# Performance work log

Measured on AMD Instinct MI355X. Metric: run time of the kernel, lower is better.

The kernel has to match this reference:

```python
import jax, jax.numpy as jnp
import numpy as np

NEG_SLOPE = 0.2  # PyG GATConv default LeakyReLU slope
EPS = 1e-16      # PyG softmax denominator epsilon


def _gat_layer(x, src, dst, W, a_src, a_dst, b, H, C):
    """One PyG-style GATConv layer (eval mode, add_self_loops already applied).
    x: [N, F_in], W: [F_in, H*C], a_src/a_dst: [H, C], b: [H*C]."""
    N = x.shape[0]
    h = (x @ W).reshape(N, H, C)                       # [N,H,C]
    alpha_src = jnp.sum(h * a_src, axis=-1)            # [N,H]
    alpha_dst = jnp.sum(h * a_dst, axis=-1)            # [N,H]
    e = jax.nn.leaky_relu(alpha_src[src] + alpha_dst[dst], NEG_SLOPE)  # [E,H]
    m = jax.ops.segment_max(e, dst, num_segments=N)    # [N,H] segment-softmax max
    p = jnp.exp(e - m[dst])                            # [E,H]
    s = jax.ops.segment_sum(p, dst, num_segments=N)    # [N,H]
    attn = p / (s[dst] + EPS)                          # [E,H]
    out = jax.ops.segment_sum(attn[:, :, None] * h[src], dst, num_segments=N)  # [N,H,C]
    return out.reshape(N, H * C) + b


def _add_self_loops(edge_index, N):
    loop = jnp.arange(N, dtype=edge_index.dtype)
    src = jnp.concatenate([edge_index[0], loop])
    dst = jnp.concatenate([edge_index[1], loop])
    return src, dst


def setup_inputs() -> dict:
    key = jax.random.key(0)
    N, E = 50000, 500000
    F_in, H, C = 336, 4, 128
    HC = H * C  # 512
    n_cls = 10
    ks = jax.random.split(key, 16)

    def glorot(k, shape):
        fan = shape[0] + shape[-1]
        return jax.random.normal(k, shape, jnp.float32) * jnp.sqrt(2.0 / fan)

    x = jax.random.normal(ks[0], (N, F_in), jnp.float32)
    edge_index = jax.random.randint(ks[1], (2, E), 0, N, dtype=jnp.int64)
    return {
        "x": x,
        "edge_index": edge_index,
        "W1": glorot(ks[2], (F_in, HC)),
        "a_src1": glorot(ks[3], (H, C)),
        "a_dst1": glorot(ks[4], (H, C)),
        "b1": jnp.zeros((HC,), jnp.float32),
        "W2": glorot(ks[5], (HC, HC)),
        "a_src2": glorot(ks[6], (H, C)),
        "a_dst2": glorot(ks[7], (H, C)),
        "b2": jnp.zeros((HC,), jnp.float32),
        "Wc1": glorot(ks[8], (HC, C)),
        "bc1": jnp.zeros((C,), jnp.float32),
        "Wc2": glorot(ks[9], (C, n_cls)),
        "bc2": jnp.zeros((n_cls,), jnp.float32),
    }


def reference(x, edge_index, W1, a_src1, a_dst1, b1, W2, a_src2, a_dst2, b2, Wc1, bc1, Wc2, bc2):
    H, C = 4, 128
    N = x.shape[0]
    src, dst = _add_self_loops(edge_index, N)
    h = _gat_layer(x, src, dst, W1, a_src1, a_dst1, b1, H, C)
    h = jax.nn.elu(h)  # ELU between layers only
    h = _gat_layer(h, src, dst, W2, a_src2, a_dst2, b2, H, C)
    # classifier (dropout is identity in eval)
    z = jax.nn.relu(h @ Wc1 + bc1)
    logits = z @ Wc2 + bc2
    return logits
```

## Files before the change

kernel.cpp:

```cpp
#include <hip/hip_runtime.h>
#include <math.h>

typedef unsigned short u16;
typedef unsigned int u32;
typedef short short8 __attribute__((ext_vector_type(8)));
typedef __bf16 bf16x8 __attribute__((ext_vector_type(8)));
typedef float f32x4 __attribute__((ext_vector_type(4)));
typedef u32 u32x4 __attribute__((ext_vector_type(4)));

typedef const __attribute__((address_space(1))) void* as1cv;
typedef __attribute__((address_space(3))) void* as3v;

__device__ __forceinline__ void gload16(const void* g, void* l) {
    __builtin_amdgcn_global_load_lds((as1cv)g, (as3v)l, 16, 0, 0);
}

__device__ __forceinline__ float b2f(u16 u) {
    union { u32 i; float f; } v; v.i = ((u32)u) << 16; return v.f;
}
__device__ __forceinline__ float b2f_lo(u32 q) {
    union { u32 i; float f; } v; v.i = q << 16; return v.f;
}
__device__ __forceinline__ float b2f_hi(u32 q) {
    union { u32 i; float f; } v; v.i = q & 0xffff0000u; return v.f;
}
__device__ __forceinline__ u16 f2b(float f) {
    union { float f; u32 i; } v; v.f = f;
    u32 i = v.i;
    u32 r = (i + 0x7fffu + ((i >> 16) & 1u)) >> 16;
    return (u16)r;
}
__device__ __forceinline__ u32 pack2(u16 a, u16 b) { return (u32)a | ((u32)b << 16); }


__device__ void agg_dev(const int* __restrict__ rowptr, const int* __restrict__ col,
                        const float* __restrict__ asrc, const float* __restrict__ adst,
                        const u16* __restrict__ hb, const float* __restrict__ bias,
                        u16* __restrict__ outb, int elu, int NODES) {
    const int wid = __builtin_amdgcn_readfirstlane((blockIdx.x * 256 + threadIdx.x) >> 6);
    const int nwaves = gridDim.x << 2;
    const int l = threadIdx.x & 63;
    const int hd = l >> 4;
    const int cbase = 8 * l;
    float bv[8];
#pragma unroll
    for (int c = 0; c < 8; c++) bv[c] = bias[cbase + c];

    for (int n = wid; n < NODES; n += nwaves) {
        const int beg = __builtin_amdgcn_readfirstlane(rowptr[n]);
        const int end = __builtin_amdgcn_readfirstlane(rowptr[n + 1]);
        const float ad = adst[n * 4 + hd];
        float acc0[8], acc1[8];
#pragma unroll
        for (int c = 0; c < 8; c++) { acc0[c] = 0.f; acc1[c] = 0.f; }
        float ss0 = 0.f, ss1 = 0.f;
        for (int j = beg; j < end; j += 8) {
            int s[8];
#pragma unroll
            for (int q = 0; q < 8; q++) {
                int jq = j + q;
                jq = jq < end ? jq : end - 1;
                s[q] = __builtin_amdgcn_readfirstlane(col[jq]);
            }
            u32x4 g[8];
#pragma unroll
            for (int q = 0; q < 8; q++)
                g[q] = *(const u32x4*)(hb + (size_t)s[q] * 512 + cbase);
            float p[8];
#pragma unroll
            for (int q = 0; q < 8; q++) {
                float e = asrc[(size_t)s[q] * 4 + hd] + ad;
                e = e > 0.f ? e : 0.2f * e;
                float pe = __expf(e);
                p[q] = (j + q < end) ? pe : 0.f;
            }
#pragma unroll
            for (int q = 0; q < 8; q += 2) {
                ss0 += p[q]; ss1 += p[q + 1];
#pragma unroll
                for (int u = 0; u < 4; u++) {
                    acc0[2 * u]     += p[q]     * b2f_lo(g[q][u]);
                    acc0[2 * u + 1] += p[q]     * b2f_hi(g[q][u]);
                    acc1[2 * u]     += p[q + 1] * b2f_lo(g[q + 1][u]);
                    acc1[2 * u + 1] += p[q + 1] * b2f_hi(g[q + 1][u]);
                }
            }
        }
        float inv = 1.f / (ss0 + ss1 + 1e-16f);
        float v[8];
#pragma unroll
        for (int c = 0; c < 8; c++) {
            float tv = (acc0[c] + acc1[c]) * inv + bv[c];
            if (elu) tv = tv > 0.f ? tv : expm1f(tv);
            v[c] = tv;
        }
        u32x4 ov;
        ov[0] = pack2(f2b(v[0]), f2b(v[1]));
        ov[1] = pack2(f2b(v[2]), f2b(v[3]));
        ov[2] = pack2(f2b(v[4]), f2b(v[5]));
        ov[3] = pack2(f2b(v[6]), f2b(v[7]));
        *(u32x4*)(outb + (size_t)n * 512 + cbase) = ov;
    }
}

__device__ void gemm_dev(const u16* __restrict__ A, const u16* __restrict__ Bt,
                         u16* __restrict__ C, const float* __restrict__ bias,
                         const float* __restrict__ aS, const float* __restrict__ aD,
                         float* __restrict__ asr, float* __restrict__ ads,
                         const float* __restrict__ Wc2, const float* __restrict__ bc2,
                         float* __restrict__ outp,
                         int M, int N, int K, int act, char* shm,
                         u16* As0, u16* As1, u16* Bs0, u16* Bs1,
                         float (*red)[128][2]) {
    const int t = threadIdx.x;
    const int l = t & 63, w = t >> 6;

    const int nwg = gridDim.x * gridDim.y;
    const int fid = blockIdx.x + gridDim.x * blockIdx.y;
    int logical;
    {
        const int q = nwg >> 3, r = nwg & 7;
        const int xcd = fid & 7, ix = fid >> 3;
        logical = (xcd < r ? xcd * (q + 1) : r * (q + 1) + (xcd - r) * q) + ix;
    }
    const int gy = gridDim.y;
    const int mtile = logical / gy;
    const int hd_ = logical - mtile * gy;
    const int m0 = mtile * 128, n0 = hd_ * 128;

    const int wm = (w >> 1) * 64, wn = (w & 1) * 64;

    const int rl0 = w * 32 + (l >> 2);
    const int rl1 = rl0 + 16;
    const int gso = 8 * ((l & 3) ^ ((l >> 3) & 3));
    const u16* pA0 = A + (size_t)min(m0 + rl0, M - 1) * K + gso;
    const u16* pA1 = A + (size_t)min(m0 + rl1, M - 1) * K + gso;
    const u16* pB0 = Bt + (size_t)min(n0 + rl0, N - 1) * K + gso;
    const u16* pB1 = Bt + (size_t)min(n0 + rl1, N - 1) * K + gso;
    const int wbase = (w * 32) * 32;

    const int rs = ((l & 15) >> 1) & 3;
    const int roff = 8 * ((l >> 4) ^ rs);

    f32x4 acc[4][4];
    f32x4 z4 = {0.f, 0.f, 0.f, 0.f};
#pragma unroll
    for (int i = 0; i < 4; i++)
#pragma unroll
        for (int j = 0; j < 4; j++) acc[i][j] = z4;

    auto STAGE = [&](u16* As_, u16* Bs_, int k0) {
        gload16(pA0 + k0, As_ + wbase);
        gload16(pA1 + k0, As_ + wbase + 16 * 32);
        gload16(pB0 + k0, Bs_ + wbase);
        gload16(pB1 + k0, Bs_ + wbase + 16 * 32);
    };
    auto COMP = [&](const u16* As_, const u16* Bs_) {
        bf16x8 af[4], bfr[4];
#pragma unroll
        for (int i = 0; i < 4; i++) {
            af[i]  = *(const bf16x8*)(As_ + (wm + i * 16 + (l & 15)) * 32 + roff);
            bfr[i] = *(const bf16x8*)(Bs_ + (wn + i * 16 + (l & 15)) * 32 + roff);
        }
        __builtin_amdgcn_s_setprio(1);
#pragma unroll
        for (int i = 0; i < 4; i++)
#pragma unroll
            for (int j = 0; j < 4; j++)
                acc[i][j] = __builtin_amdgcn_mfma_f32_16x16x32_bf16(af[i], bfr[j], acc[i][j], 0, 0, 0);
        __builtin_amdgcn_s_setprio(0);
    };

    const int ns = K >> 5;
    STAGE(As0, Bs0, 0);
    __syncthreads();
    int s = 0;
    while (true) {
        if (s + 1 < ns) STAGE(As1, Bs1, (s + 1) << 5);
        COMP(As0, Bs0);
        __syncthreads();
        if (++s >= ns) break;
        if (s + 1 < ns) STAGE(As0, Bs0, (s + 1) << 5);
        COMP(As1, Bs1);
        __syncthreads();
        if (++s >= ns) break;
    }

    if (act == 2) {
        float* wl = (float*)shm;
        float (*logbuf)[128][10] = (float (*)[128][10])(shm + 8192);
        for (int i = t; i < 1280; i += 256) wl[i] = Wc2[i];
        if (t < 10) wl[1280 + t] = bc2[t];
        __syncthreads();
        int cj[4];
#pragma unroll
        for (int j = 0; j < 4; j++) cj[j] = wn + j * 16 + (l & 15);
#pragma unroll
        for (int i = 0; i < 4; i++) {
#pragma unroll
            for (int r = 0; r < 4; r++) {
                float zv[4];
#pragma unroll
                for (int j = 0; j < 4; j++) {
                    float v = acc[i][j][r] + (bias ? bias[cj[j]] : 0.f);
                    zv[j] = v > 0.f ? v : 0.f;
                }
                float part[10];
#pragma unroll
                for (int k = 0; k < 10; k++) {
                    float s2 = 0.f;
#pragma unroll
                    for (int j = 0; j < 4; j++) s2 += zv[j] * wl[cj[j] * 10 + k];
#pragma unroll
                    for (int o = 1; o < 16; o <<= 1) s2 += __shfl_xor(s2, o);
                    part[k] = s2;
                }
                if ((l & 15) == 0) {
                    int rl = wm + i * 16 + (l >> 4) * 4 + r;
#pragma unroll
                    for (int k = 0; k < 10; k++) logbuf[w & 1][rl][k] = part[k];
                }
            }
        }
        __syncthreads();
        if (t < 128) {
            int row = m0 + t;
            if (row < M) {
#pragma unroll
                for (int k = 0; k < 10; k++)
                    outp[(size_t)row * 10 + k] =
                        logbuf[0][t][k] + logbuf[1][t][k] + wl[1280 + k];
            }
        }
        return;
    }

#pragma unroll
    for (int i = 0; i < 4; i++) {
        int rbase = m0 + wm + i * 16 + (l >> 4) * 4;
#pragma unroll
        for (int j = 0; j < 4; j++) {
            int c = n0 + wn + j * 16 + (l & 15);
            float bv = bias ? bias[c] : 0.f;
#pragma unroll
            for (int r = 0; r < 4; r++) {
                int row = rbase + r;
                if (row < M) {
                    float v = acc[i][j][r] + bv;
                    if (act == 1) v = v > 0.f ? v : 0.f;
                    C[(size_t)row * N + c] = f2b(v);
                }
            }
        }
    }

    if (aS) {
        const int hd = n0 >> 7;
        float aSv[4], aDv[4];
#pragma unroll
        for (int j = 0; j < 4; j++) {
            int c = n0 + wn + j * 16 + (l & 15);
            aSv[j] = aS[c];
            aDv[j] = aD[c];
        }
#pragma unroll
        for (int i = 0; i < 4; i++) {
#pragma unroll
            for (int r = 0; r < 4; r++) {
                float vs = 0.f, vd = 0.f;
#pragma unroll
                for (int j = 0; j < 4; j++) {
                    float hv = acc[i][j][r];
                    vs += hv * aSv[j];
                    vd += hv * aDv[j];
                }
#pragma unroll
                for (int o = 1; o < 16; o <<= 1) {
                    vs += __shfl_xor(vs, o);
                    vd += __shfl_xor(vd, o);
                }
                if ((l & 15) == 0) {
                    int rl = wm + i * 16 + (l >> 4) * 4 + r;
                    red[w & 1][rl][0] = vs;
                    red[w & 1][rl][1] = vd;
                }
            }
        }
        __syncthreads();
        if (t < 128) {
            int row = m0 + t;
            if (row < M) {
                asr[row * 4 + hd] = red[0][t][0] + red[1][t][0];
                ads[row * 4 + hd] = red[0][t][1] + red[1][t][1];
            }
        }
    }
}

__global__ __launch_bounds__(256) void BaselineGAT_41764261987077_kernel(
    int phase, int aux,
    const float* x, const int* ei,
    const float* W1, const float* as1, const float* ad1, const float* b1,
    const float* W2, const float* as2, const float* ad2, const float* b2,
    const float* Wc1, const float* bc1, const float* Wc2, const float* bc2,
    float* out,
    u16* hAb, u16* hbB, float* asr, float* ads,
    u16* xb, u16* w1t, u16* w2t, u16* wc1t,
    int* flag, int* cnt, int* tmp, int* bsum, int* boff,
    int* rowptr, int* cursor, int* col,
    const u16* gA, const u16* gB, u16* gC, const float* gBias,
    const float* gAs, const float* gAd,
    int gM, int gN, int gK, int gAct,
    int NODES, int E, int nblk)
{
    __shared__ f32x4 shm4[2176];
    char* shm = (char*)shm4;
    u16* As0 = (u16*)shm;
    u16* As1 = (u16*)(shm + 8192);
    u16* Bs0 = (u16*)(shm + 16384);
    u16* Bs1 = (u16*)(shm + 24576);
    float (*red)[128][2] = (float (*)[128][2])(shm + 32768);
    int* smi = (int*)shm;
    int* smb = (int*)(shm + 2048);

    const int t = threadIdx.x;
    const int gid = blockIdx.x * 256 + t;
    const int EN = E + NODES;

    switch (phase) {
    case 100: {
        if (gid < NODES * 10) out[gid] = 1000.0f;
    } break;
    case 0: {
        if (blockIdx.x == 0) {
            if (t == 0) smi[256] = 0;
            __syncthreads();
            for (int j = t; j < 1024; j += 256)
                if (ei[2 * j + 1] != 0) atomicAdd(&smi[256], 1);
            __syncthreads();
            if (t == 0) flag[0] = (smi[256] < 16) ? 2 : 1;
        } else {
            int i = (blockIdx.x - 1) * 256 + t;
            if (i < NODES) cnt[i] = 0;
        }
    } break;
    case 2: {
        if (gid >= EN) return;
        int step = flag[0];
        int d;
        if (gid < E) {
            d = ei[(size_t)(E + gid) * step];
            if ((unsigned)d >= (unsigned)NODES) d = 0;
        } else d = gid - E;
        atomicAdd(&cnt[d], 1);
    } break;
    case 3: {
        smi[t] = (gid < NODES) ? cnt[gid] : 0;
        __syncthreads();
        for (int o = 1; o < 256; o <<= 1) {
            int add = (t >= o) ? smi[t - o] : 0;
            __syncthreads();
            smi[t] += add;
            __syncthreads();
        }
        if (gid < NODES) tmp[gid] = smi[t];
        if (t == 255) bsum[blockIdx.x] = smi[255];
    } break;
    case 5: {
        smb[t] = (t < nblk) ? bsum[t] : 0;
        __syncthreads();
        for (int o = 1; o < 256; o <<= 1) {
            int add = (t >= o) ? smb[t - o] : 0;
            __syncthreads();
            smb[t] += add;
            __syncthreads();
        }
        int base = (blockIdx.x == 0) ? 0 : smb[blockIdx.x - 1];
        if (gid >= NODES) return;
        int incl = tmp[gid] + base;
        rowptr[gid + 1] = incl;
        cursor[gid] = incl - cnt[gid];
        if (gid == 0) rowptr[0] = 0;
    } break;
    case 6: {
        if (gid >= EN) return;
        int step = flag[0];
        int d, s;
        if (gid < E) {
            s = ei[(size_t)gid * step];
            d = ei[(size_t)(E + gid) * step];
            if ((unsigned)s >= (unsigned)NODES) s = 0;
            if ((unsigned)d >= (unsigned)NODES) d = 0;
        } else { d = gid - E; s = d; }
        int pos = atomicAdd(&cursor[d], 1);
        col[pos] = s;
    } break;
    case 20: {
        int i = gid;
        const int XC = NODES * 44;
        if (i < XC) {
            int n = i / 44, kk = (i - n * 44) * 8;
            short8 o;
            if (kk < 336) {
                const f32x4* xp = (const f32x4*)(x + (size_t)n * 336 + kk);
                f32x4 f0 = xp[0], f1 = xp[1];
                o[0] = (short)f2b(f0[0]); o[1] = (short)f2b(f0[1]);
                o[2] = (short)f2b(f0[2]); o[3] = (short)f2b(f0[3]);
                o[4] = (short)f2b(f1[0]); o[5] = (short)f2b(f1[1]);
                o[6] = (short)f2b(f1[2]); o[7] = (short)f2b(f1[3]);
            } else {
#pragma unroll
                for (int e = 0; e < 8; e++) o[e] = 0;
            }
            *(short8*)(xb + (size_t)n * 352 + kk) = o;
            return;
        }
        i -= XC;
        if (i < 512 * 352) {
            int n = i / 352, k = i - n * 352;
            w1t[i] = (k < 336) ? f2b(W1[(size_t)k * 512 + n]) : (u16)0;
            return;
        }
        i -= 512 * 352;
        if (i < 512 * 512) {
            int n = i >> 9, k = i & 511;
            w2t[i] = f2b(W2[(size_t)k * 512 + n]);
            return;
        }
        i -= 512 * 512;
        if (i < 128 * 512) {
            int n = i >> 9, k = i & 511;
            wc1t[i] = f2b(Wc1[(size_t)k * 128 + n]);
        }
    } break;
    case 30: gemm_dev(gA, gB, gC, gBias, gAs, gAd, asr, ads,
                      Wc2, bc2, out, gM, gN, gK, gAct, shm,
                      As0, As1, Bs0, Bs1, red); break;
    case 31: agg_dev(rowptr, col, asr, ads, hAb, gBias, hbB, aux, NODES); break;
    }
}

extern "C" void kernel_launch(void* const* d_in, const int* in_sizes, int n_in,
                              void* d_out, int out_size, void* d_ws, size_t ws_size,
                              hipStream_t stream) {
    const float* x   = (const float*)d_in[0];
    const int*   ei  = (const int*)d_in[1];
    const float* W1  = (const float*)d_in[2];
    const float* as1 = (const float*)d_in[3];
    const float* ad1 = (const float*)d_in[4];
    const float* b1  = (const float*)d_in[5];
    const float* W2  = (const float*)d_in[6];
    const float* as2 = (const float*)d_in[7];
    const float* ad2 = (const float*)d_in[8];
    const float* b2  = (const float*)d_in[9];
    const float* Wc1 = (const float*)d_in[10];
    const float* bc1 = (const float*)d_in[11];
    const float* Wc2 = (const float*)d_in[12];
    const float* bc2 = (const float*)d_in[13];

    const int NODES = in_sizes[0] / 336;
    const int E     = in_sizes[1] / 2;

    char* ws = (char*)d_ws;
    size_t off = 0;
    auto alloc = [&](size_t b) -> char* {
        char* p = ws + off; off = (off + b + 255) & ~(size_t)255; return p;
    };
    u16*   xb   = (u16*)alloc((size_t)NODES * 352 * 2);
    u16*   hAb  = (u16*)alloc((size_t)NODES * 512 * 2);
    u16*   hbB  = (u16*)alloc((size_t)NODES * 512 * 2);
    float* asr  = (float*)alloc((size_t)NODES * 4 * 4);
    float* ads  = (float*)alloc((size_t)NODES * 4 * 4);
    u16*   w1t  = (u16*)alloc((size_t)512 * 352 * 2);
    u16*   w2t  = (u16*)alloc((size_t)512 * 512 * 2);
    u16*   wc1t = (u16*)alloc((size_t)128 * 512 * 2);
    int* flag   = (int*)alloc(256);
    int* cnt    = (int*)alloc((size_t)NODES * 4);
    int* tmp    = (int*)alloc((size_t)NODES * 4);
    int* bsum   = (int*)alloc(4096);
    int* boff   = (int*)alloc(4096);
    int* rowptr = (int*)alloc((size_t)(NODES + 1) * 4);
    int* cursor = (int*)alloc((size_t)NODES * 4);
    int* col    = (int*)alloc((size_t)(E + NODES) * 4);

    const int nblk = (NODES + 255) / 256;
    const int eblk = (E + NODES + 255) / 256;
    const int oblk = (out_size + 255) / 256;
    const int mt   = (NODES + 127) / 128;
    const int cvt_total = NODES * 44 + 512 * 352 + 512 * 512 + 128 * 512;

    auto L = [&](int phase, int aux, dim3 grid,
                 const u16* gA = nullptr, const u16* gB = nullptr,
                 u16* gC = nullptr, const float* gBias = nullptr,
                 const float* gAs = nullptr, const float* gAd = nullptr,
                 int gM = 0, int gN = 0, int gK = 0, int gAct = 0) {
        BaselineGAT_41764261987077_kernel<<<grid, 256, 0, stream>>>(
            phase, aux, x, ei, W1, as1, ad1, b1, W2, as2, ad2, b2,
            Wc1, bc1, Wc2, bc2, (float*)d_out,
            hAb, hbB, asr, ads, xb, w1t, w2t, wc1t,
            flag, cnt, tmp, bsum, boff, rowptr, cursor, col,
            gA, gB, gC, gBias, gAs, gAd, gM, gN, gK, gAct,
            NODES, E, nblk);
    };

    if (n_in < 14 || off > ws_size) { L(100, 1, oblk); return; }

    L(0, 0, nblk + 1);
    L(2, 0, eblk);
    L(3, 0, nblk);
    L(5, 0, nblk);
    L(6, 0, eblk);

    L(20, 0, (cvt_total + 255) / 256);

    L(30, 0, dim3(mt, 4), xb, w1t, hAb, nullptr, as1, ad1, NODES, 512, 352, 0);
    L(31, 1, 4096, nullptr, nullptr, nullptr, b1);

    L(30, 0, dim3(mt, 4), hbB, w2t, hAb, nullptr, as2, ad2, NODES, 512, 512, 0);
    L(31, 0, 4096, nullptr, nullptr, nullptr, b2);

    L(30, 0, dim3(mt, 1), hbB, wc1t, nullptr, bc1, nullptr, nullptr, NODES, 128, 512, 2);
}
```

Before: 576.5 us.

## Triple-buffer GEMM K-loop with vmcnt-based waits and dynamic shared memory

```diff
diff --git a/kernel.cpp b/kernel.cpp
--- a/kernel.cpp
+++ b/kernel.cpp
@@ -109,11 +109,16 @@
                          float* __restrict__ asr, float* __restrict__ ads,
                          const float* __restrict__ Wc2, const float* __restrict__ bc2,
                          float* __restrict__ outp,
-                         int M, int N, int K, int act, char* shm,
-                         u16* As0, u16* As1, u16* Bs0, u16* Bs1,
-                         float (*red)[128][2]) {
+                         int M, int N, int K, int act, char* shm) {
     const int t = threadIdx.x;
     const int l = t & 63, w = t >> 6;
+
+    u16* As0 = (u16*)shm;
+    u16* As1 = (u16*)(shm + 8192);
+    u16* As2 = (u16*)(shm + 16384);
+    u16* Bs0 = (u16*)(shm + 24576);
+    u16* Bs1 = (u16*)(shm + 32768);
+    u16* Bs2 = (u16*)(shm + 40960);
 
     const int nwg = gridDim.x * gridDim.y;
     const int fid = blockIdx.x + gridDim.x * blockIdx.y;
@@ -170,19 +175,30 @@
                 acc[i][j] = __builtin_amdgcn_mfma_f32_16x16x32_bf16(af[i], bfr[j], acc[i][j], 0, 0, 0);
         __builtin_amdgcn_s_setprio(0);
     };
+    auto WSEL = [&](int s_, int ns_) {
+        int ahead = ns_ - 1 - s_;
+        if (ahead >= 2)      asm volatile("s_waitcnt vmcnt(8)" ::: "memory");
+        else if (ahead == 1) asm volatile("s_waitcnt vmcnt(4)" ::: "memory");
+        else                 asm volatile("s_waitcnt vmcnt(0)" ::: "memory");
+    };
 
     const int ns = K >> 5;
     STAGE(As0, Bs0, 0);
-    __syncthreads();
+    STAGE(As1, Bs1, 32);
+    STAGE(As2, Bs2, 64);
     int s = 0;
     while (true) {
-        if (s + 1 < ns) STAGE(As1, Bs1, (s + 1) << 5);
-        COMP(As0, Bs0);
-        __syncthreads();
+        WSEL(s, ns); __builtin_amdgcn_s_barrier();
+        COMP(As0, Bs0); __builtin_amdgcn_s_barrier();
+        if (s + 3 < ns) STAGE(As0, Bs0, (s + 3) << 5);
         if (++s >= ns) break;
-        if (s + 1 < ns) STAGE(As0, Bs0, (s + 1) << 5);
-        COMP(As1, Bs1);
-        __syncthreads();
+        WSEL(s, ns); __builtin_amdgcn_s_barrier();
+        COMP(As1, Bs1); __builtin_amdgcn_s_barrier();
+        if (s + 3 < ns) STAGE(As1, Bs1, (s + 3) << 5);
+        if (++s >= ns) break;
+        WSEL(s, ns); __builtin_amdgcn_s_barrier();
+        COMP(As2, Bs2); __builtin_amdgcn_s_barrier();
+        if (s + 3 < ns) STAGE(As2, Bs2, (s + 3) << 5);
         if (++s >= ns) break;
     }
 
@@ -255,6 +271,7 @@
     }
 
     if (aS) {
+        float (*red)[128][2] = (float (*)[128][2])shm;
         const int hd = n0 >> 7;
         float aSv[4], aDv[4];
 #pragma unroll
@@ -313,15 +330,10 @@
     int gM, int gN, int gK, int gAct,
     int NODES, int E, int nblk)
 {
-    __shared__ f32x4 shm4[2176];
-    char* shm = (char*)shm4;
-    u16* As0 = (u16*)shm;
-    u16* As1 = (u16*)(shm + 8192);
-    u16* Bs0 = (u16*)(shm + 16384);
-    u16* Bs1 = (u16*)(shm + 24576);
-    float (*red)[128][2] = (float (*)[128][2])(shm + 32768);
-    int* smi = (int*)shm;
-    int* smb = (int*)(shm + 2048);
+    __shared__ int sstat[1024];
+    extern __shared__ char dynshm[];
+    int* smi = sstat;
+    int* smb = sstat + 512;
 
     const int t = threadIdx.x;
     const int gid = blockIdx.x * 256 + t;
@@ -434,8 +446,7 @@
         }
     } break;
     case 30: gemm_dev(gA, gB, gC, gBias, gAs, gAd, asr, ads,
-                      Wc2, bc2, out, gM, gN, gK, gAct, shm,
-                      As0, As1, Bs0, Bs1, red); break;
+                      Wc2, bc2, out, gM, gN, gK, gAct, dynshm); break;
     case 31: agg_dev(rowptr, col, asr, ads, hAb, gBias, hbB, aux, NODES); break;
     }
 }
@@ -489,12 +500,12 @@
     const int mt   = (NODES + 127) / 128;
     const int cvt_total = NODES * 44 + 512 * 352 + 512 * 512 + 128 * 512;
 
-    auto L = [&](int phase, int aux, dim3 grid,
+    auto L = [&](int phase, int aux, dim3 grid, size_t shmem,
                  const u16* gA = nullptr, const u16* gB = nullptr,
                  u16* gC = nullptr, const float* gBias = nullptr,
                  const float* gAs = nullptr, const float* gAd = nullptr,
                  int gM = 0, int gN = 0, int gK = 0, int gAct = 0) {
-        BaselineGAT_41764261987077_kernel<<<grid, 256, 0, stream>>>(
+        BaselineGAT_41764261987077_kernel<<<grid, 256, shmem, stream>>>(
             phase, aux, x, ei, W1, as1, ad1, b1, W2, as2, ad2, b2,
             Wc1, bc1, Wc2, bc2, (float*)d_out,
             hAb, hbB, asr, ads, xb, w1t, w2t, wc1t,
@@ -502,22 +513,23 @@
             gA, gB, gC, gBias, gAs, gAd, gM, gN, gK, gAct,
             NODES, E, nblk);
     };
-
-    if (n_in < 14 || off > ws_size) { L(100, 1, oblk); return; }
-
-    L(0, 0, nblk + 1);
-    L(2, 0, eblk);
-    L(3, 0, nblk);
-    L(5, 0, nblk);
-    L(6, 0, eblk);
-
-    L(20, 0, (cvt_total + 255) / 256);
-
-    L(30, 0, dim3(mt, 4), xb, w1t, hAb, nullptr, as1, ad1, NODES, 512, 352, 0);
-    L(31, 1, 4096, nullptr, nullptr, nullptr, b1);
-
-    L(30, 0, dim3(mt, 4), hbB, w2t, hAb, nullptr, as2, ad2, NODES, 512, 512, 0);
-    L(31, 0, 4096, nullptr, nullptr, nullptr, b2);
-
-    L(30, 0, dim3(mt, 1), hbB, wc1t, nullptr, bc1, nullptr, nullptr, NODES, 128, 512, 2);
-}
+    const size_t GSH = 49152;
+
+    if (n_in < 14 || off > ws_size) { L(100, 1, oblk, 0); return; }
+
+    L(0, 0, nblk + 1, 0);
+    L(2, 0, eblk, 0);
+    L(3, 0, nblk, 0);
+    L(5, 0, nblk, 0);
+    L(6, 0, eblk, 0);
+
+    L(20, 0, (cvt_total + 255) / 256, 0);
+
+    L(30, 0, dim3(mt, 4), GSH, xb, w1t, hAb, nullptr, as1, ad1, NODES, 512, 352, 0);
+    L(31, 1, 4096, 0, nullptr, nullptr, nullptr, b1);
+
+    L(30, 0, dim3(mt, 4), GSH, hbB, w2t, hAb, nullptr, as2, ad2, NODES, 512, 512, 0);
+    L(31, 0, 4096, 0, nullptr, nullptr, nullptr, b2);
+
+    L(30, 0, dim3(mt, 1), GSH, hbB, wc1t, nullptr, bc1, nullptr, nullptr, NODES, 128, 512, 2);
+}
```

New measurement: 571.8 us. No clear change (-0.8%).
